# Kernel tuning notes

Measured on AMD Instinct MI355X. Metric: run time of the kernel, lower is better.

Reference implementation:

```python
import jax, jax.numpy as jnp
import numpy as np

B, S, D = 64, 256, 768   # batch, max_seq_length, bert hidden
CAP = 8                  # semantic_cap_size (= num_capsules)
NT = 10                  # ntasks (= num_routes)
TASK = 5
NUM_ITER = 3


def squash(t, axis=-1):
    sq = jnp.sum(t * t, axis=axis, keepdims=True)
    return (sq / (1.0 + sq)) * t / jnp.sqrt(sq)


def setup_inputs() -> dict:
    key = jax.random.key(0)
    k0, k1, k2, k3 = jax.random.split(key, 4)
    x = jax.random.normal(k0, (B, S, D), dtype=jnp.float32)
    # per-task semantic projections: ntasks x Linear(768 -> CAP)
    fc1_w = jax.random.normal(k1, (NT, CAP, D), dtype=jnp.float32) * 0.02
    fc1_b = jnp.zeros((NT, CAP), dtype=jnp.float32)
    # route_weights: [num_capsules, num_routes, in_channel=S*CAP, class_dim=S]
    route_weights = jax.random.normal(k2, (CAP, NT, S * CAP, S), dtype=jnp.float32)
    # larger: Linear(CAP -> 768)
    larger_w = jax.random.normal(k3, (D, CAP), dtype=jnp.float32) * 0.02
    larger_b = jnp.zeros((D,), dtype=jnp.float32)
    return {"x": x, "task": TASK, "fc1_w": fc1_w, "fc1_b": fc1_b,
            "route_weights": route_weights, "larger_w": larger_w, "larger_b": larger_b}


def reference(x, task, fc1_w, fc1_b, route_weights, larger_w, larger_b):
    Bb, Ss, _ = x.shape
    nt, cap, _ = fc1_w.shape
    # --- semantic capsules: per-task Linear, cat over task dim, squash over tasks ---
    sem = jnp.einsum('bsd,ncd->bscn', x, fc1_w) + fc1_b.T[None, None]  # [B,S,CAP,NT]
    sem = sem.reshape(Bb, Ss * cap, nt)          # matches torch view(B,-1,1)+cat
    sem = squash(sem, axis=-1)
    u = jnp.transpose(sem, (0, 2, 1))            # [B, NT, S*CAP] (transpose(2,1))
    # --- tsv capsules: dynamic routing ---
    priors = jnp.einsum('brk,crkl->cbrl', u, route_weights)[:, :, :, None, :]  # [CAP,B,NT,1,S]
    tsv = jnp.tril(jnp.ones((nt, nt), dtype=x.dtype))
    tsv_t = tsv[task].reshape(1, 1, nt, 1, 1)
    mask = jnp.where(tsv[task] == 0, jnp.float32(-10000.0), jnp.float32(0.0)).reshape(1, 1, nt, 1, 1)
    logits = jnp.zeros_like(priors)
    vote = None
    for i in range(NUM_ITER):
        logits = logits * tsv_t + mask
        probs = jax.nn.softmax(logits, axis=2)                     # softmax over routes
        vote = jnp.sum(probs * priors, axis=2, keepdims=True)      # [CAP,B,1,1,S]
        out = squash(vote, axis=-1)
        if i != NUM_ITER - 1:
            logits = logits + jnp.sum(priors * out, axis=-1, keepdims=True)
    # torch .view on contiguous [CAP,B,1,1,S] -> (B, S, CAP): row-major reinterpret
    h = vote.reshape(-1).reshape(Bb, Ss, cap)
    return h @ larger_w.T + larger_b
```

## Files before the change

### kernel.cpp

```cpp
#include <hip/hip_runtime.h>
#include <hip/hip_bf16.h>

#define Bq 64
#define Sq 256
#define Dq 768
#define CAPq 8
#define NTq 10
#define SCq 2048

typedef short bf16x8 __attribute__((ext_vector_type(8)));
typedef float f32x4  __attribute__((ext_vector_type(4)));

static __device__ __forceinline__ short bfhi(float f) {
    return (short)(__float_as_uint(f) >> 16);
}
static __device__ __forceinline__ short bflo(float f) {
    float hi = __uint_as_float(__float_as_uint(f) & 0xFFFF0000u);
    return (short)(__float_as_uint(f - hi) >> 16);
}

__global__ __launch_bounds__(256) void k0_cvt(const float* __restrict__ w,
                                              short* __restrict__ hi,
                                              short* __restrict__ lo) {
    int i = blockIdx.x * 256 + threadIdx.x;
    if (i < NTq * CAPq * Dq) {
        int k8 = i / 640;
        int rem = i - k8 * 640;
        int o = rem >> 3, kf = rem & 7;
        float f = w[o * Dq + k8 * 8 + kf];
        hi[i] = bfhi(f);
        lo[i] = bflo(f);
    }
}

__device__ __forceinline__ void k1_comp(const float* xv, const short* pwh, const short* pwl,
                                        int ko80, f32x4* acc) {
    bf16x8 ah, al;
#pragma unroll
    for (int i = 0; i < 8; ++i) { ah[i] = bfhi(xv[i]); al[i] = bflo(xv[i]); }
#pragma unroll
    for (int f = 0; f < 5; ++f) {
        bf16x8 bh = *reinterpret_cast<const bf16x8*>(pwh + ko80 + f * 128);
        bf16x8 bl = *reinterpret_cast<const bf16x8*>(pwl + ko80 + f * 128);
        acc[f] = __builtin_amdgcn_mfma_f32_16x16x32_bf16(al, bh, acc[f], 0, 0, 0);
        acc[f] = __builtin_amdgcn_mfma_f32_16x16x32_bf16(ah, bl, acc[f], 0, 0, 0);
        acc[f] = __builtin_amdgcn_mfma_f32_16x16x32_bf16(ah, bh, acc[f], 0, 0, 0);
    }
}

__global__ __launch_bounds__(256) void k1_sem(const float* __restrict__ x,
                                              const short* __restrict__ fwh,
                                              const short* __restrict__ fwl,
                                              const float* __restrict__ fc1b,
                                              short* __restrict__ u_hi,
                                              short* __restrict__ u_lo) {
    __shared__ float redS[3][20][64];
    const int t = threadIdx.x;
    const int L = t & 63, w = t >> 6;
    const int colL = L & 15, kg = L >> 4;
    const int rowA = blockIdx.x * 16 + colL;

    f32x4 acc[5];
#pragma unroll
    for (int f = 0; f < 5; ++f) acc[f] = (f32x4){0.f, 0.f, 0.f, 0.f};

    const float* px = x + (size_t)rowA * Dq + w * 192 + kg * 8;
    const short* pwh = fwh + kg * 640 + colL * 8;
    const short* pwl = fwl + kg * 640 + colL * 8;

    float xv0[8], xv1[8];
    *reinterpret_cast<float4*>(&xv0[0]) = *reinterpret_cast<const float4*>(px);
    *reinterpret_cast<float4*>(&xv0[4]) = *reinterpret_cast<const float4*>(px + 4);

    for (int kc = 0; kc < 192; kc += 64) {
        {
            const float* p = px + kc + 32;
            *reinterpret_cast<float4*>(&xv1[0]) = *reinterpret_cast<const float4*>(p);
            *reinterpret_cast<float4*>(&xv1[4]) = *reinterpret_cast<const float4*>(p + 4);
        }
        __builtin_amdgcn_sched_barrier(0);
        k1_comp(xv0, pwh, pwl, (w * 192 + kc) * 80, acc);
        __builtin_amdgcn_sched_barrier(0);
        {
            int kn = (kc + 64 < 192) ? kc + 64 : 0;
            const float* p = px + kn;
            *reinterpret_cast<float4*>(&xv0[0]) = *reinterpret_cast<const float4*>(p);
            *reinterpret_cast<float4*>(&xv0[4]) = *reinterpret_cast<const float4*>(p + 4);
        }
        __builtin_amdgcn_sched_barrier(0);
        k1_comp(xv1, pwh, pwl, (w * 192 + kc + 32) * 80, acc);
        __builtin_amdgcn_sched_barrier(0);
    }

    if (w > 0) {
#pragma unroll
        for (int f = 0; f < 5; ++f)
#pragma unroll
            for (int g = 0; g < 4; ++g)
                redS[w - 1][f * 4 + g][L] = acc[f][g];
    }
    __syncthreads();
    if (w == 0) {
        float bias[5];
#pragma unroll
        for (int f = 0; f < 5; ++f) bias[f] = fc1b[f * 16 + colL];
        const int cc = colL & 7;
        const int npar = (colL >> 3) & 1;
#pragma unroll
        for (int reg = 0; reg < 4; ++reg) {
            const int row = blockIdx.x * 16 + kg * 4 + reg;
            const int b = row >> 8, s = row & 255;
            float v[5], sqp = 0.f;
#pragma unroll
            for (int f = 0; f < 5; ++f) {
                v[f] = acc[f][reg] + redS[0][f * 4 + reg][L] + redS[1][f * 4 + reg][L]
                     + redS[2][f * 4 + reg][L] + bias[f];
                sqp = fmaf(v[f], v[f], sqp);
            }
            float sq = sqp + __shfl_xor(sqp, 8, 64);
            float scale = (sq / (1.f + sq)) / sqrtf(sq);
#pragma unroll
            for (int f = 0; f < 5; ++f) {
                int n = 2 * f + npar;
                size_t off = (((size_t)n * 256 + s) * 64 + b) * 8 + cc;
                float val = v[f] * scale;
                u_hi[off] = bfhi(val);
                u_lo[off] = bflo(val);
            }
        }
    }
}

__device__ __forceinline__ void k2_comp2(const float2* bv, const short* puh, const short* pul,
                                         int ao, f32x4* accE, f32x4* accO) {
    bf16x8 bhE, blE, bhO, blO;
#pragma unroll
    for (int i = 0; i < 8; ++i) {
        bhE[i] = bfhi(bv[i].x); blE[i] = bflo(bv[i].x);
        bhO[i] = bfhi(bv[i].y); blO[i] = bflo(bv[i].y);
    }
#pragma unroll
    for (int m = 0; m < 4; ++m) {
        bf16x8 ah = *reinterpret_cast<const bf16x8*>(puh + ao + m * 128);
        bf16x8 al = *reinterpret_cast<const bf16x8*>(pul + ao + m * 128);
        accE[m] = __builtin_amdgcn_mfma_f32_16x16x32_bf16(al, bhE, accE[m], 0, 0, 0);
        accE[m] = __builtin_amdgcn_mfma_f32_16x16x32_bf16(ah, blE, accE[m], 0, 0, 0);
        accE[m] = __builtin_amdgcn_mfma_f32_16x16x32_bf16(ah, bhE, accE[m], 0, 0, 0);
        accO[m] = __builtin_amdgcn_mfma_f32_16x16x32_bf16(al, bhO, accO[m], 0, 0, 0);
        accO[m] = __builtin_amdgcn_mfma_f32_16x16x32_bf16(ah, blO, accO[m], 0, 0, 0);
        accO[m] = __builtin_amdgcn_mfma_f32_16x16x32_bf16(ah, bhO, accO[m], 0, 0, 0);
    }
}

__global__ __launch_bounds__(256, 3) void k2_priors(const short* __restrict__ u_hi,
                                                    const short* __restrict__ u_lo,
                                                    const float* __restrict__ rw,
                                                    const int* __restrict__ task_p,
                                                    float* __restrict__ part) {
    const int r = blockIdx.y;
    if (r > *task_p) return;
    __shared__ float redS[3][2][16][64];
    const int t = threadIdx.x;
    const int L = t & 63, kh = t >> 6;
    const int colL = L & 15, kg = L >> 4;
    const int lq = blockIdx.x & 7, ks = blockIdx.x >> 3;
    const int c = blockIdx.z;
    const int le = lq * 32 + 2 * colL;
    const int kw0 = ks * 1024 + kh * 256;
    const int s00 = kw0 >> 3;

    f32x4 accE[4], accO[4];
#pragma unroll
    for (int m = 0; m < 4; ++m) {
        accE[m] = (f32x4){0.f, 0.f, 0.f, 0.f};
        accO[m] = (f32x4){0.f, 0.f, 0.f, 0.f};
    }

    const float* pb = rw + ((size_t)(c * NTq + r) * SCq + kw0 + kg * 8) * Sq + le;
    const short* puh = u_hi + (((size_t)r * 256 + s00 + kg) * 64 + colL) * 8;
    const short* pul = u_lo + (((size_t)r * 256 + s00 + kg) * 64 + colL) * 8;

    float2 bv0[8], bv1[8];
#pragma unroll
    for (int i = 0; i < 8; ++i) bv0[i] = *reinterpret_cast<const float2*>(pb + (size_t)i * Sq);

    for (int kc = 0; kc < 256; kc += 64) {
        {
            const float* p = pb + (size_t)(kc + 32) * Sq;
#pragma unroll
            for (int i = 0; i < 8; ++i) bv1[i] = *reinterpret_cast<const float2*>(p + (size_t)i * Sq);
        }
        __builtin_amdgcn_sched_barrier(0);
        k2_comp2(bv0, puh, pul, kc * 64, accE, accO);
        __builtin_amdgcn_sched_barrier(0);
        {
            int kn = (kc + 64 < 256) ? kc + 64 : 0;
            const float* p = pb + (size_t)kn * Sq;
#pragma unroll
            for (int i = 0; i < 8; ++i) bv0[i] = *reinterpret_cast<const float2*>(p + (size_t)i * Sq);
        }
        __builtin_amdgcn_sched_barrier(0);
        k2_comp2(bv1, puh, pul, (kc + 32) * 64, accE, accO);
        __builtin_amdgcn_sched_barrier(0);
    }

    if (kh > 0) {
#pragma unroll
        for (int m = 0; m < 4; ++m)
#pragma unroll
            for (int g = 0; g < 4; ++g) {
                redS[kh - 1][0][m * 4 + g][L] = accE[m][g];
                redS[kh - 1][1][m * 4 + g][L] = accO[m][g];
            }
    }
    __syncthreads();
    if (kh == 0) {
#pragma unroll
        for (int m = 0; m < 4; ++m) {
#pragma unroll
            for (int g = 0; g < 4; ++g) {
                float vE = accE[m][g] + redS[0][0][m * 4 + g][L]
                         + redS[1][0][m * 4 + g][L] + redS[2][0][m * 4 + g][L];
                float vO = accO[m][g] + redS[0][1][m * 4 + g][L]
                         + redS[1][1][m * 4 + g][L] + redS[2][1][m * 4 + g][L];
                int bb = m * 16 + kg * 4 + g;
                size_t idx = (size_t)ks * 1310720 + ((size_t)(c * Bq + bb) * NTq + r) * Sq + le;
                float2 vv; vv.x = vE; vv.y = vO;
                *reinterpret_cast<float2*>(part + idx) = vv;
            }
        }
    }
}

__global__ __launch_bounds__(256) void k34_route_out(const float* __restrict__ part,
                                                     const int* __restrict__ task_p,
                                                     const float* __restrict__ lw,
                                                     const float* __restrict__ lb,
                                                     float* __restrict__ out) {
    const int t = threadIdx.x;
    const int lane = t & 63, w = t >> 6;
    const int b = blockIdx.x & 63, c = blockIdx.x >> 6;
    const int task = *task_p;

    float pr[NTq][4];
    const float* p0 = part + ((size_t)(c * Bq + b) * NTq) * Sq + lane * 4;
#pragma unroll
    for (int r = 0; r < NTq; ++r) {
        f32x4 a = *reinterpret_cast<const f32x4*>(p0 + r * Sq);
        f32x4 d = *reinterpret_cast<const f32x4*>(p0 + 1310720 + r * Sq);
#pragma unroll
        for (int ii = 0; ii < 4; ++ii) pr[r][ii] = a[ii] + d[ii];
    }

    float logits[NTq];
#pragma unroll
    for (int r = 0; r < NTq; ++r) logits[r] = 0.f;
    float vote[4];

    for (int it = 0; it < 3; ++it) {
        float m = -1e30f;
#pragma unroll
        for (int r = 0; r < NTq; ++r) if (r <= task) m = fmaxf(m, logits[r]);
        float p[NTq]; float s = 0.f;
#pragma unroll
        for (int r = 0; r < NTq; ++r) {
            p[r] = (r <= task) ? expf(logits[r] - m) : 0.f;
            s += p[r];
        }
        float inv = 1.f / s;
#pragma unroll
        for (int ii = 0; ii < 4; ++ii) vote[ii] = 0.f;
#pragma unroll
        for (int r = 0; r < NTq; ++r) {
            float pw = p[r] * inv;
#pragma unroll
            for (int ii = 0; ii < 4; ++ii) vote[ii] = fmaf(pw, pr[r][ii], vote[ii]);
        }
        if (it == 2) break;

        float vals[11];
#pragma unroll
        for (int r = 0; r < NTq; ++r) {
            float d = 0.f;
#pragma unroll
            for (int ii = 0; ii < 4; ++ii) d = fmaf(pr[r][ii], vote[ii], d);
            vals[r] = d;
        }
        {
            float d = 0.f;
#pragma unroll
            for (int ii = 0; ii < 4; ++ii) d = fmaf(vote[ii], vote[ii], d);
            vals[10] = d;
        }
#pragma unroll
        for (int o = 32; o > 0; o >>= 1) {
#pragma unroll
            for (int v = 0; v < 11; ++v) vals[v] += __shfl_xor(vals[v], o, 64);
        }
        float sq = vals[10];
        float scale = (sq / (1.f + sq)) / sqrtf(sq);
#pragma unroll
        for (int r = 0; r < NTq; ++r)
            if (r <= task) logits[r] += scale * vals[r];
    }

    float v[8][8];
#pragma unroll
    for (int j = 0; j < 8; ++j) {
        int s0 = w * 16 + 2 * j;
#pragma unroll
        for (int ii = 0; ii < 4; ++ii) v[j][ii]     = __shfl(vote[ii], s0, 64);
#pragma unroll
        for (int ii = 0; ii < 4; ++ii) v[j][4 + ii] = __shfl(vote[ii], s0 + 1, 64);
    }
    const int rbase = c * 2048 + b * 32 + w * 8;
#pragma unroll
    for (int dd = 0; dd < 12; ++dd) {
        int d = lane + dd * 64;
        float4 wa = *reinterpret_cast<const float4*>(lw + (size_t)d * 8);
        float4 wb = *reinterpret_cast<const float4*>(lw + (size_t)d * 8 + 4);
        float lbv = lb[d];
#pragma unroll
        for (int j = 0; j < 8; ++j) {
            float acc = lbv;
            acc = fmaf(v[j][0], wa.x, acc);
            acc = fmaf(v[j][1], wa.y, acc);
            acc = fmaf(v[j][2], wa.z, acc);
            acc = fmaf(v[j][3], wa.w, acc);
            acc = fmaf(v[j][4], wb.x, acc);
            acc = fmaf(v[j][5], wb.y, acc);
            acc = fmaf(v[j][6], wb.z, acc);
            acc = fmaf(v[j][7], wb.w, acc);
            out[(size_t)(rbase + j) * Dq + d] = acc;
        }
    }
}

extern "C" void kernel_launch(void* const* d_in, const int* in_sizes, int n_in,
                              void* d_out, int out_size, void* d_ws, size_t ws_size,
                              hipStream_t stream) {
    const float* x    = (const float*)d_in[0];
    const int*   task = (const int*)d_in[1];
    const float* fc1w = (const float*)d_in[2];
    const float* fc1b = (const float*)d_in[3];
    const float* rw   = (const float*)d_in[4];
    const float* lw   = (const float*)d_in[5];
    const float* lb   = (const float*)d_in[6];
    float* out = (float*)d_out;

    short* u_hi = (short*)d_ws;
    short* u_lo = u_hi + 1310720;
    float* part = (float*)((char*)d_ws + 5242880);
    short* fwh  = (short*)((char*)d_ws + 16252928);
    short* fwl  = fwh + 61440;

    k0_cvt<<<240, 256, 0, stream>>>(fc1w, fwh, fwl);
    k1_sem<<<1024, 256, 0, stream>>>(x, fwh, fwl, fc1b, u_hi, u_lo);
    dim3 g2(16, NTq, CAPq);
    k2_priors<<<g2, 256, 0, stream>>>(u_hi, u_lo, rw, task, part);
    k34_route_out<<<512, 256, 0, stream>>>(part, task, lw, lb, out);
}
```

Measured before the change: 77.86 us.

## Stage x tile in LDS as split bf16 and flatten priors grid ordering

k1_sem now loads the whole 16x768 x tile cooperatively with coalesced float4 reads, converts it once to hi/lo bf16 in shared memory, and feeds the MFMAs from LDS instead of each lane doing strided global loads and per-iteration conversion. The shared buffer is reused for the cross-wave reduction. k2_priors switches from a 3D grid to a flat 1D grid with a custom block-index decode that interleaves k-split halves and routes/capsules, changing block scheduling order and early-exit distribution. It costs more LDS per block (48KB) and an extra barrier.

```diff
diff --git a/kernel.cpp b/kernel.cpp
--- a/kernel.cpp
+++ b/kernel.cpp
@@ -33,71 +33,66 @@
     }
 }
 
-__device__ __forceinline__ void k1_comp(const float* xv, const short* pwh, const short* pwl,
-                                        int ko80, f32x4* acc) {
-    bf16x8 ah, al;
-#pragma unroll
-    for (int i = 0; i < 8; ++i) { ah[i] = bfhi(xv[i]); al[i] = bflo(xv[i]); }
-#pragma unroll
-    for (int f = 0; f < 5; ++f) {
-        bf16x8 bh = *reinterpret_cast<const bf16x8*>(pwh + ko80 + f * 128);
-        bf16x8 bl = *reinterpret_cast<const bf16x8*>(pwl + ko80 + f * 128);
-        acc[f] = __builtin_amdgcn_mfma_f32_16x16x32_bf16(al, bh, acc[f], 0, 0, 0);
-        acc[f] = __builtin_amdgcn_mfma_f32_16x16x32_bf16(ah, bl, acc[f], 0, 0, 0);
-        acc[f] = __builtin_amdgcn_mfma_f32_16x16x32_bf16(ah, bh, acc[f], 0, 0, 0);
-    }
-}
-
 __global__ __launch_bounds__(256) void k1_sem(const float* __restrict__ x,
                                               const short* __restrict__ fwh,
                                               const short* __restrict__ fwl,
                                               const float* __restrict__ fc1b,
                                               short* __restrict__ u_hi,
                                               short* __restrict__ u_lo) {
-    __shared__ float redS[3][20][64];
+    __shared__ short xsh[12288];
+    __shared__ short xsl[12288];
     const int t = threadIdx.x;
     const int L = t & 63, w = t >> 6;
     const int colL = L & 15, kg = L >> 4;
-    const int rowA = blockIdx.x * 16 + colL;
+    const int R0 = blockIdx.x * 16;
+
+    const float* xbase = x + (size_t)R0 * Dq;
+#pragma unroll
+    for (int i = 0; i < 12; ++i) {
+        int li = t + i * 256;
+        int r = li / 192, j = li - r * 192;
+        float4 v = *reinterpret_cast<const float4*>(xbase + (size_t)r * Dq + j * 4);
+        int k8 = j >> 1, kf = (j & 1) * 4;
+        int off = (k8 * 16 + r) * 8 + kf;
+        short4 h4, l4;
+        h4.x = bfhi(v.x); h4.y = bfhi(v.y); h4.z = bfhi(v.z); h4.w = bfhi(v.w);
+        l4.x = bflo(v.x); l4.y = bflo(v.y); l4.z = bflo(v.z); l4.w = bflo(v.w);
+        *reinterpret_cast<short4*>(&xsh[off]) = h4;
+        *reinterpret_cast<short4*>(&xsl[off]) = l4;
+    }
+    __syncthreads();
 
     f32x4 acc[5];
 #pragma unroll
     for (int f = 0; f < 5; ++f) acc[f] = (f32x4){0.f, 0.f, 0.f, 0.f};
 
-    const float* px = x + (size_t)rowA * Dq + w * 192 + kg * 8;
     const short* pwh = fwh + kg * 640 + colL * 8;
     const short* pwl = fwl + kg * 640 + colL * 8;
 
-    float xv0[8], xv1[8];
-    *reinterpret_cast<float4*>(&xv0[0]) = *reinterpret_cast<const float4*>(px);
-    *reinterpret_cast<float4*>(&xv0[4]) = *reinterpret_cast<const float4*>(px + 4);
-
-    for (int kc = 0; kc < 192; kc += 64) {
-        {
-            const float* p = px + kc + 32;
-            *reinterpret_cast<float4*>(&xv1[0]) = *reinterpret_cast<const float4*>(p);
-            *reinterpret_cast<float4*>(&xv1[4]) = *reinterpret_cast<const float4*>(p + 4);
-        }
-        __builtin_amdgcn_sched_barrier(0);
-        k1_comp(xv0, pwh, pwl, (w * 192 + kc) * 80, acc);
-        __builtin_amdgcn_sched_barrier(0);
-        {
-            int kn = (kc + 64 < 192) ? kc + 64 : 0;
-            const float* p = px + kn;
-            *reinterpret_cast<float4*>(&xv0[0]) = *reinterpret_cast<const float4*>(p);
-            *reinterpret_cast<float4*>(&xv0[4]) = *reinterpret_cast<const float4*>(p + 4);
-        }
-        __builtin_amdgcn_sched_barrier(0);
-        k1_comp(xv1, pwh, pwl, (w * 192 + kc + 32) * 80, acc);
-        __builtin_amdgcn_sched_barrier(0);
-    }
-
+#pragma unroll 2
+    for (int kc = 0; kc < 192; kc += 32) {
+        const int k8 = ((w * 192 + kc) >> 3) + kg;
+        bf16x8 ah = *reinterpret_cast<const bf16x8*>(&xsh[(k8 * 16 + colL) * 8]);
+        bf16x8 al = *reinterpret_cast<const bf16x8*>(&xsl[(k8 * 16 + colL) * 8]);
+        const int ko80 = (w * 192 + kc) * 80;
+#pragma unroll
+        for (int f = 0; f < 5; ++f) {
+            bf16x8 bh = *reinterpret_cast<const bf16x8*>(pwh + ko80 + f * 128);
+            bf16x8 bl = *reinterpret_cast<const bf16x8*>(pwl + ko80 + f * 128);
+            acc[f] = __builtin_amdgcn_mfma_f32_16x16x32_bf16(al, bh, acc[f], 0, 0, 0);
+            acc[f] = __builtin_amdgcn_mfma_f32_16x16x32_bf16(ah, bl, acc[f], 0, 0, 0);
+            acc[f] = __builtin_amdgcn_mfma_f32_16x16x32_bf16(ah, bh, acc[f], 0, 0, 0);
+        }
+    }
+
+    float* redS = reinterpret_cast<float*>(xsh);
+    __syncthreads();
     if (w > 0) {
 #pragma unroll
         for (int f = 0; f < 5; ++f)
 #pragma unroll
             for (int g = 0; g < 4; ++g)
-                redS[w - 1][f * 4 + g][L] = acc[f][g];
+                redS[((w - 1) * 20 + f * 4 + g) * 64 + L] = acc[f][g];
     }
     __syncthreads();
     if (w == 0) {
@@ -108,13 +103,14 @@
         const int npar = (colL >> 3) & 1;
 #pragma unroll
         for (int reg = 0; reg < 4; ++reg) {
-            const int row = blockIdx.x * 16 + kg * 4 + reg;
+            const int row = R0 + kg * 4 + reg;
             const int b = row >> 8, s = row & 255;
             float v[5], sqp = 0.f;
 #pragma unroll
             for (int f = 0; f < 5; ++f) {
-                v[f] = acc[f][reg] + redS[0][f * 4 + reg][L] + redS[1][f * 4 + reg][L]
-                     + redS[2][f * 4 + reg][L] + bias[f];
+                v[f] = acc[f][reg] + redS[(0 * 20 + f * 4 + reg) * 64 + L]
+                     + redS[(1 * 20 + f * 4 + reg) * 64 + L]
+                     + redS[(2 * 20 + f * 4 + reg) * 64 + L] + bias[f];
                 sqp = fmaf(v[f], v[f], sqp);
             }
             float sq = sqp + __shfl_xor(sqp, 8, 64);
@@ -157,14 +153,18 @@
                                                     const float* __restrict__ rw,
                                                     const int* __restrict__ task_p,
                                                     float* __restrict__ part) {
-    const int r = blockIdx.y;
+    const int bid = blockIdx.x;
+    const int lq = bid / 160;
+    const int rem = bid - lq * 160;
+    const int ks = rem & 1;
+    const int rc = rem >> 1;
+    const int c = rc / 10;
+    const int r = rc - c * 10;
     if (r > *task_p) return;
     __shared__ float redS[3][2][16][64];
     const int t = threadIdx.x;
     const int L = t & 63, kh = t >> 6;
     const int colL = L & 15, kg = L >> 4;
-    const int lq = blockIdx.x & 7, ks = blockIdx.x >> 3;
-    const int c = blockIdx.z;
     const int le = lq * 32 + 2 * colL;
     const int kw0 = ks * 1024 + kh * 256;
     const int s00 = kw0 >> 3;
@@ -356,7 +356,6 @@
 
     k0_cvt<<<240, 256, 0, stream>>>(fc1w, fwh, fwl);
     k1_sem<<<1024, 256, 0, stream>>>(x, fwh, fwl, fc1b, u_hi, u_lo);
-    dim3 g2(16, NTq, CAPq);
-    k2_priors<<<g2, 256, 0, stream>>>(u_hi, u_lo, rw, task, part);
+    k2_priors<<<1280, 256, 0, stream>>>(u_hi, u_lo, rw, task, part);
     k34_route_out<<<512, 256, 0, stream>>>(part, task, lw, lb, out);
 }
```

Measured after the change: 76.23 us. 2.1% less time.
